# Optimization experiments

Hardware: AMD Instinct MI355X
Metric: run time of the kernel (lower is better)

Reference implementation:

```python
import jax, jax.numpy as jnp
import numpy as np

NEG_INF = -1e30

def setup_inputs() -> dict:
    key = jax.random.key(0)
    k1, k2, k3 = jax.random.split(key, 3)
    B, H, S, D = 2, 16, 2048, 128
    q = jax.random.normal(k1, (B, H, S, D), dtype=jnp.float32)
    k = jax.random.normal(k2, (B, H, S, D), dtype=jnp.float32)
    v = jax.random.normal(k3, (B, H, S, D), dtype=jnp.float32)
    return {"q": q, "k": k, "v": v}

def reference(q, k, v):
    # F.scaled_dot_product_attention(q, k, v, is_causal=True), MATH backend:
    # full score matrix, causal mask (top-left aligned: j <= i), softmax, bmm.
    D = q.shape[-1]
    scale = 1.0 / jnp.sqrt(jnp.asarray(D, dtype=q.dtype))
    scores = jnp.einsum('bhqd,bhkd->bhqk', q, k) * scale  # [B,H,S,S]
    Sq, Sk = scores.shape[-2], scores.shape[-1]
    causal = jnp.arange(Sk)[None, :] <= jnp.arange(Sq)[:, None]  # [Sq,Sk]
    scores = jnp.where(causal[None, None], scores, NEG_INF)
    attn = jax.nn.softmax(scores, axis=-1)
    return jnp.einsum('bhqk,bhkd->bhqd', attn, v)
```

## Files before the change

kernel.cpp:

```cpp
#include <hip/hip_runtime.h>
#include <cstdint>
#include <cstddef>

typedef __attribute__((ext_vector_type(8))) short short8;
typedef __attribute__((ext_vector_type(4))) float floatx4;
typedef __attribute__((ext_vector_type(2))) unsigned int uint2v;

namespace {
constexpr int kBH  = 32;
constexpr int kS   = 2048;
constexpr int kD   = 128;
constexpr int kBQ  = 64;
constexpr int kBK  = 64;
constexpr int kNQT = kS / kBQ;
constexpr int PST  = 72;
constexpr size_t kKVElems = (size_t)kBH * kS * kD;
}

__device__ __forceinline__ unsigned short f32_bf16(float f) {
    union { float f; unsigned u; } c; c.f = f;
    unsigned u = c.u;
    u += 0x7FFFu + ((u >> 16) & 1u);
    return (unsigned short)(u >> 16);
}

__device__ __forceinline__ unsigned cvt_pk_bf16(float lo, float hi) {
    unsigned r;
    asm("v_cvt_pk_bf16_f32 %0, %1, %2" : "=v"(r) : "v"(lo), "v"(hi));
    return r;
}

__device__ __forceinline__ unsigned pack_bf16x2(float lo, float hi) {
    return cvt_pk_bf16(lo, hi);
}

__device__ __forceinline__ float fast_exp2(float x) {
#if __has_builtin(__builtin_amdgcn_exp2f)
    return __builtin_amdgcn_exp2f(x);
#else
    return __expf(x * 0.6931471805599453f);
#endif
}

__device__ __forceinline__ void gl_lds16(const void* g, void* l) {
    __builtin_amdgcn_global_load_lds(
        (const __attribute__((address_space(1))) unsigned int*)g,
        (__attribute__((address_space(3))) unsigned int*)l, 16, 0, 0);
}

__global__ __launch_bounds__(256)
void prepass(const float* __restrict__ K, const float* __restrict__ V,
             unsigned short* __restrict__ Kb, unsigned short* __restrict__ Vt) {
    const int b = (int)blockIdx.x;
    const int t = (int)threadIdx.x;
    if (b < 4096) {
        const size_t i0 = ((size_t)b * 256 + t) * 8;
        floatx4 a = *(const floatx4*)(K + i0);
        floatx4 c = *(const floatx4*)(K + i0 + 4);
        union { unsigned u[4]; short8 v; } pk;
        pk.u[0] = cvt_pk_bf16(a[0], a[1]);
        pk.u[1] = cvt_pk_bf16(a[2], a[3]);
        pk.u[2] = cvt_pk_bf16(c[0], c[1]);
        pk.u[3] = cvt_pk_bf16(c[2], c[3]);
        *(short8*)(Kb + i0) = pk.v;
    } else {
        __shared__ float ldsT[64][68];
        const int vb = b - 4096;
        const int bh = vb >> 6;
        const int rem = vb & 63;
        const int s0 = (rem >> 1) * 64;
        const int d0 = (rem & 1) * 64;
        const float* vbase = V + ((size_t)bh * kS + s0) * kD + d0;
        const int sr = t >> 4, c4 = (t & 15) * 4;
#pragma unroll
        for (int p = 0; p < 4; ++p) {
            const int s = p * 16 + sr;
            *(floatx4*)&ldsT[s][c4] = *(const floatx4*)(vbase + (size_t)s * kD + c4);
        }
        __syncthreads();
        const int dr = t >> 2, sc = (t & 3) * 16;
        union { unsigned u[8]; short8 v[2]; } pk;
#pragma unroll
        for (int j = 0; j < 8; ++j)
            pk.u[j] = cvt_pk_bf16(ldsT[sc + 2 * j][dr], ldsT[sc + 2 * j + 1][dr]);
        unsigned short* out = Vt + ((size_t)(bh * kD + d0 + dr)) * kS + s0 + sc;
        *(short8*)out = pk.v[0];
        *(short8*)(out + 8) = pk.v[1];
    }
}


struct TileState {
    short8  qf[4];
    floatx4 oacc[8];
    float   lsum[4];
};

__device__ __forceinline__ void tile_step(
    TileState& ts, const unsigned short* kT, const unsigned short* vT,
    unsigned short* pw, int l16, int quad, int rowl, bool doMask)
{
    floatx4 sacc[4];
    __builtin_amdgcn_s_setprio(1);
#pragma unroll
    for (int nt = 0; nt < 4; ++nt) {
        floatx4 acc = (floatx4){0.f, 0.f, 0.f, 0.f};
#pragma unroll
        for (int ks = 0; ks < 4; ++ks) {
            short8 kf = *(const short8*)&kT[(nt * 16 + l16) * 128 + (((ks * 4 + quad) ^ l16) << 3)];
            acc = __builtin_amdgcn_mfma_f32_16x16x32_bf16(ts.qf[ks], kf, acc, 0, 0, 0);
        }
        sacc[nt] = acc;
    }
    __builtin_amdgcn_s_setprio(0);

    if (doMask) {
#pragma unroll
        for (int nt = 0; nt < 4; ++nt) {
            const int col = nt * 16 + l16;
#pragma unroll
            for (int r = 0; r < 4; ++r)
                if (col > rowl + r) sacc[nt][r] = -1e30f;
        }
    }

#pragma unroll
    for (int nt = 0; nt < 4; ++nt)
#pragma unroll
        for (int r = 0; r < 4; ++r)
            sacc[nt][r] = fast_exp2(sacc[nt][r]);
#pragma unroll
    for (int r = 0; r < 4; ++r)
        ts.lsum[r] += (sacc[0][r] + sacc[1][r]) + (sacc[2][r] + sacc[3][r]);

#pragma unroll
    for (int r = 0; r < 4; ++r) {
#pragma unroll
        for (int np = 0; np < 2; ++np) {
            const unsigned u = cvt_pk_bf16(sacc[np * 2][r], sacc[np * 2 + 1][r]);
            pw[(quad * 4 + r) * PST + (np * 2) * 16 + l16]     = (unsigned short)u;
            pw[(quad * 4 + r) * PST + (np * 2 + 1) * 16 + l16] = (unsigned short)(u >> 16);
        }
    }

    short8 pf[2];
#pragma unroll
    for (int ks = 0; ks < 2; ++ks)
        pf[ks] = *(const short8*)&pw[l16 * PST + ks * 32 + quad * 8];

    __builtin_amdgcn_s_setprio(1);
#pragma unroll
    for (int nd = 0; nd < 8; ++nd) {
        floatx4 acc = ts.oacc[nd];
#pragma unroll
        for (int ks = 0; ks < 2; ++ks) {
            short8 vf = *(const short8*)&vT[(nd * 16 + l16) * 64 + ((((ks * 4 + quad)) ^ (l16 & 7)) << 3)];
            acc = __builtin_amdgcn_mfma_f32_16x16x32_bf16(pf[ks], vf, acc, 0, 0, 0);
        }
        ts.oacc[nd] = acc;
    }
    __builtin_amdgcn_s_setprio(0);
}

__global__ __launch_bounds__(256, 2)
void fa_fwd_ws(const float* __restrict__ Qg, const unsigned short* __restrict__ Kb,
               const unsigned short* __restrict__ Vt, float* __restrict__ Og) {
    const int id = (int)blockIdx.x;
    const int qA = id >> 5;
    const int qB = kNQT - 1 - qA;
    const int bh = id & (kBH - 1);
    const int t    = (int)threadIdx.x;
    const int wave = t >> 6;
    const int lane = t & 63;
    const int quad = lane >> 4;
    const int l16  = lane & 15;
    const int rowl = wave * 16 + quad * 4;

    __shared__ __align__(16) unsigned short kT0[kBK * 128];
    __shared__ __align__(16) unsigned short kT1[kBK * 128];
    __shared__ __align__(16) unsigned short vT0[kD * 64];
    __shared__ __align__(16) unsigned short vT1[kD * 64];
    __shared__ __align__(16) unsigned short pT[4 * 16 * PST];
    unsigned short* pw = &pT[wave * 16 * PST];

    const float scale = 0.12751744459649126f;

    TileState A, B;
#pragma unroll
    for (int i = 0; i < 8; ++i) { A.oacc[i] = (floatx4){0,0,0,0}; B.oacc[i] = (floatx4){0,0,0,0}; }
#pragma unroll
    for (int r = 0; r < 4; ++r) { A.lsum[r] = 0.f; B.lsum[r] = 0.f; }

    {
        const float* qpA = Qg + ((size_t)bh * kS + qA * kBQ + wave * 16 + l16) * kD;
        const float* qpB = Qg + ((size_t)bh * kS + qB * kBQ + wave * 16 + l16) * kD;
#pragma unroll
        for (int ks = 0; ks < 4; ++ks) {
            const int d0 = ks * 32 + quad * 8;
            floatx4 a0 = *(const floatx4*)(qpA + d0);
            floatx4 a1 = *(const floatx4*)(qpA + d0 + 4);
            floatx4 b0 = *(const floatx4*)(qpB + d0);
            floatx4 b1 = *(const floatx4*)(qpB + d0 + 4);
            union { unsigned u[4]; short8 v; } pa, pb;
            pa.u[0] = cvt_pk_bf16(a0[0] * scale, a0[1] * scale);
            pa.u[1] = cvt_pk_bf16(a0[2] * scale, a0[3] * scale);
            pa.u[2] = cvt_pk_bf16(a1[0] * scale, a1[1] * scale);
            pa.u[3] = cvt_pk_bf16(a1[2] * scale, a1[3] * scale);
            pb.u[0] = cvt_pk_bf16(b0[0] * scale, b0[1] * scale);
            pb.u[1] = cvt_pk_bf16(b0[2] * scale, b0[3] * scale);
            pb.u[2] = cvt_pk_bf16(b1[0] * scale, b1[1] * scale);
            pb.u[3] = cvt_pk_bf16(b1[2] * scale, b1[3] * scale);
            A.qf[ks] = pa.v;
            B.qf[ks] = pb.v;
        }
    }

    const unsigned short* kBase = Kb + (size_t)bh * kS * kD;
    const unsigned short* vBase = Vt + (size_t)bh * kD * kS;

    auto stage = [&](int kt, unsigned short* kDst, unsigned short* vDst) {
        const int kj0 = kt * kBK;
        const int rbase = wave * 16;
#pragma unroll
        for (int i = 0; i < 4; ++i) {
            const int row = rbase + i * 4 + (lane >> 4);
            const int cg  = (lane & 15) ^ (row & 15);
            gl_lds16(kBase + ((size_t)(kj0 + row)) * kD + cg * 8,
                     &kDst[(rbase + i * 4) * 128]);
        }
        const int dbase = wave * 32;
#pragma unroll
        for (int i = 0; i < 4; ++i) {
            const int d  = dbase + i * 8 + (lane >> 3);
            const int cg = (lane & 7) ^ (d & 7);
            gl_lds16(vBase + (size_t)d * kS + kj0 + cg * 8,
                     &vDst[(dbase + i * 8) * 64]);
        }
    };

    const int last = qB;
    stage(0, kT0, vT0);
    __syncthreads();

    int kt = 0;
    for (;;) {
        if (kt < last) stage(kt + 1, kT1, vT1);
        if (kt <= qA) tile_step(A, kT0, vT0, pw, l16, quad, rowl, kt == qA);
        tile_step(B, kT0, vT0, pw, l16, quad, rowl, kt == last);
        __syncthreads();
        if (kt == last) break;
        ++kt;
        if (kt < last) stage(kt + 1, kT0, vT0);
        if (kt <= qA) tile_step(A, kT1, vT1, pw, l16, quad, rowl, kt == qA);
        tile_step(B, kT1, vT1, pw, l16, quad, rowl, kt == last);
        __syncthreads();
        if (kt == last) break;
        ++kt;
    }

#pragma unroll
    for (int tile = 0; tile < 2; ++tile) {
        TileState& ts = tile ? B : A;
        const int qt = tile ? qB : qA;
        float ls[4];
#pragma unroll
        for (int r = 0; r < 4; ++r) ls[r] = ts.lsum[r];
#pragma unroll
        for (int off = 1; off < 16; off <<= 1)
#pragma unroll
            for (int r = 0; r < 4; ++r)
                ls[r] += __shfl_xor(ls[r], off, 64);
        float inv[4];
#pragma unroll
        for (int r = 0; r < 4; ++r) inv[r] = 1.0f / ls[r];
        float* ob = Og + ((size_t)bh * kS + qt * kBQ + wave * 16 + quad * 4) * kD;
#pragma unroll
        for (int nd = 0; nd < 8; ++nd)
#pragma unroll
            for (int r = 0; r < 4; ++r)
                ob[(size_t)r * kD + nd * 16 + l16] = ts.oacc[nd][r] * inv[r];
    }
}

namespace {
constexpr int KSTf = 136;
constexpr int VSTf = 72;
}

__device__ __forceinline__ void tile_step_f(
    TileState& ts, const unsigned short* kT, const unsigned short* vT,
    unsigned short* pw, int l16, int quad, int rowl, bool doMask)
{
    floatx4 sacc[4];
    __builtin_amdgcn_s_setprio(1);
#pragma unroll
    for (int nt = 0; nt < 4; ++nt) {
        floatx4 acc = (floatx4){0.f, 0.f, 0.f, 0.f};
#pragma unroll
        for (int ks = 0; ks < 4; ++ks) {
            short8 kf = *(const short8*)&kT[(nt * 16 + l16) * KSTf + ks * 32 + quad * 8];
            acc = __builtin_amdgcn_mfma_f32_16x16x32_bf16(ts.qf[ks], kf, acc, 0, 0, 0);
        }
        sacc[nt] = acc;
    }
    __builtin_amdgcn_s_setprio(0);
    if (doMask) {
#pragma unroll
        for (int nt = 0; nt < 4; ++nt) {
            const int col = nt * 16 + l16;
#pragma unroll
            for (int r = 0; r < 4; ++r)
                if (col > rowl + r) sacc[nt][r] = -1e30f;
        }
    }
#pragma unroll
    for (int nt = 0; nt < 4; ++nt)
#pragma unroll
        for (int r = 0; r < 4; ++r)
            sacc[nt][r] = fast_exp2(sacc[nt][r]);
#pragma unroll
    for (int r = 0; r < 4; ++r)
        ts.lsum[r] += (sacc[0][r] + sacc[1][r]) + (sacc[2][r] + sacc[3][r]);
#pragma unroll
    for (int r = 0; r < 4; ++r) {
#pragma unroll
        for (int np = 0; np < 2; ++np) {
            const unsigned u = cvt_pk_bf16(sacc[np * 2][r], sacc[np * 2 + 1][r]);
            pw[(quad * 4 + r) * PST + (np * 2) * 16 + l16]     = (unsigned short)u;
            pw[(quad * 4 + r) * PST + (np * 2 + 1) * 16 + l16] = (unsigned short)(u >> 16);
        }
    }
    short8 pf[2];
#pragma unroll
    for (int ks = 0; ks < 2; ++ks)
        pf[ks] = *(const short8*)&pw[l16 * PST + ks * 32 + quad * 8];
    __builtin_amdgcn_s_setprio(1);
#pragma unroll
    for (int nd = 0; nd < 8; ++nd) {
        floatx4 acc = ts.oacc[nd];
#pragma unroll
        for (int ks = 0; ks < 2; ++ks) {
            short8 vf = *(const short8*)&vT[(nd * 16 + l16) * VSTf + ks * 32 + quad * 8];
            acc = __builtin_amdgcn_mfma_f32_16x16x32_bf16(pf[ks], vf, acc, 0, 0, 0);
        }
        ts.oacc[nd] = acc;
    }
    __builtin_amdgcn_s_setprio(0);
}

__global__ __launch_bounds__(256, 2)
void fa_fwd_fallback(const float* __restrict__ Qg, const float* __restrict__ Kg,
                     const float* __restrict__ Vg, float* __restrict__ Og) {
    const int id = (int)blockIdx.x;
    const int qA = id >> 5;
    const int qB = kNQT - 1 - qA;
    const int bh = id & (kBH - 1);
    const int t    = (int)threadIdx.x;
    const int wave = t >> 6;
    const int lane = t & 63;
    const int quad = lane >> 4;
    const int l16  = lane & 15;
    const int rowl = wave * 16 + quad * 4;

    __shared__ __align__(16) unsigned short kT[2][kBK * KSTf];
    __shared__ __align__(16) unsigned short vT[2][kD * VSTf];
    __shared__ __align__(16) unsigned short pT[4 * 16 * PST];
    unsigned short* pw = &pT[wave * 16 * PST];

    const float scale = 0.12751744459649126f;

    TileState A, B;
#pragma unroll
    for (int i = 0; i < 8; ++i) { A.oacc[i] = (floatx4){0,0,0,0}; B.oacc[i] = (floatx4){0,0,0,0}; }
#pragma unroll
    for (int r = 0; r < 4; ++r) { A.lsum[r] = 0.f; B.lsum[r] = 0.f; }
    {
        const float* qpA = Qg + ((size_t)bh * kS + qA * kBQ + wave * 16 + l16) * kD;
        const float* qpB = Qg + ((size_t)bh * kS + qB * kBQ + wave * 16 + l16) * kD;
#pragma unroll
        for (int ks = 0; ks < 4; ++ks) {
            const int d0 = ks * 32 + quad * 8;
            floatx4 a0 = *(const floatx4*)(qpA + d0);
            floatx4 a1 = *(const floatx4*)(qpA + d0 + 4);
            floatx4 b0 = *(const floatx4*)(qpB + d0);
            floatx4 b1 = *(const floatx4*)(qpB + d0 + 4);
            union { unsigned u[4]; short8 v; } pa, pb;
            pa.u[0] = cvt_pk_bf16(a0[0] * scale, a0[1] * scale);
            pa.u[1] = cvt_pk_bf16(a0[2] * scale, a0[3] * scale);
            pa.u[2] = cvt_pk_bf16(a1[0] * scale, a1[1] * scale);
            pa.u[3] = cvt_pk_bf16(a1[2] * scale, a1[3] * scale);
            pb.u[0] = cvt_pk_bf16(b0[0] * scale, b0[1] * scale);
            pb.u[1] = cvt_pk_bf16(b0[2] * scale, b0[3] * scale);
            pb.u[2] = cvt_pk_bf16(b1[0] * scale, b1[1] * scale);
            pb.u[3] = cvt_pk_bf16(b1[2] * scale, b1[3] * scale);
            A.qf[ks] = pa.v;
            B.qf[ks] = pb.v;
        }
    }

    const int kRow8 = t >> 5;
    const int kCol4 = t & 31;
    const int vD    = t & 127;
    const int vR2   = t >> 7;
    const float* kBaseH = Kg + (size_t)bh * kS * kD;
    const float* vBaseH = Vg + (size_t)bh * kS * kD;
    floatx4 kpre[8];
    float   vpreL[16], vpreH[16];

    auto issue_kv_loads = [&](int kt) {
        const float* kb = kBaseH + (size_t)(kt * kBK) * kD;
        const float* vb = vBaseH + (size_t)(kt * kBK) * kD;
#pragma unroll
        for (int p = 0; p < 8; ++p)
            kpre[p] = *(const floatx4*)(kb + (size_t)(p * 8 + kRow8) * kD + kCol4 * 4);
#pragma unroll
        for (int p = 0; p < 16; ++p) {
            const int j = p * 2 + vR2;
            vpreL[p] = vb[(size_t)(2 * j) * kD + vD];
            vpreH[p] = vb[(size_t)(2 * j + 1) * kD + vD];
        }
    };
    auto store_kv = [&](int buf) {
#pragma unroll
        for (int p = 0; p < 8; ++p) {
            union { unsigned u[2]; uint2v v; } w;
            w.u[0] = cvt_pk_bf16(kpre[p][0], kpre[p][1]);
            w.u[1] = cvt_pk_bf16(kpre[p][2], kpre[p][3]);
            *(uint2v*)&kT[buf][(p * 8 + kRow8) * KSTf + kCol4 * 4] = w.v;
        }
#pragma unroll
        for (int p = 0; p < 16; ++p) {
            const int j = p * 2 + vR2;
            *(unsigned*)&vT[buf][vD * VSTf + 2 * j] = pack_bf16x2(vpreL[p], vpreH[p]);
        }
    };

    const int last = qB;
    issue_kv_loads(0);
    store_kv(0);
    __syncthreads();
    for (int kt = 0; kt <= last; ++kt) {
        const int buf = kt & 1;
        if (kt < last) issue_kv_loads(kt + 1);
        if (kt <= qA) tile_step_f(A, kT[buf], vT[buf], pw, l16, quad, rowl, kt == qA);
        tile_step_f(B, kT[buf], vT[buf], pw, l16, quad, rowl, kt == last);
        if (kt < last) {
            store_kv(buf ^ 1);
            __syncthreads();
        }
    }
#pragma unroll
    for (int tile = 0; tile < 2; ++tile) {
        TileState& ts = tile ? B : A;
        const int qt = tile ? qB : qA;
        float ls[4];
#pragma unroll
        for (int r = 0; r < 4; ++r) ls[r] = ts.lsum[r];
#pragma unroll
        for (int off = 1; off < 16; off <<= 1)
#pragma unroll
            for (int r = 0; r < 4; ++r)
                ls[r] += __shfl_xor(ls[r], off, 64);
        float inv[4];
#pragma unroll
        for (int r = 0; r < 4; ++r) inv[r] = 1.0f / ls[r];
        float* ob = Og + ((size_t)bh * kS + qt * kBQ + wave * 16 + quad * 4) * kD;
#pragma unroll
        for (int nd = 0; nd < 8; ++nd)
#pragma unroll
            for (int r = 0; r < 4; ++r)
                ob[(size_t)r * kD + nd * 16 + l16] = ts.oacc[nd][r] * inv[r];
    }
}

extern "C" void kernel_launch(void* const* d_in, const int* in_sizes, int n_in,
                              void* d_out, int out_size, void* d_ws, size_t ws_size,
                              hipStream_t stream) {
    (void)in_sizes; (void)n_in; (void)out_size;
    const float* q = (const float*)d_in[0];
    const float* k = (const float*)d_in[1];
    const float* v = (const float*)d_in[2];
    float* o = (float*)d_out;
    const size_t need = 2 * kKVElems * sizeof(unsigned short);
    if (ws_size >= need) {
        unsigned short* Kb = (unsigned short*)d_ws;
        unsigned short* Vt = Kb + kKVElems;
        prepass<<<dim3(4096 + 2048), 256, 0, stream>>>(k, v, Kb, Vt);
        fa_fwd_ws<<<dim3((kNQT / 2) * kBH), 256, 0, stream>>>(q, Kb, Vt, o);
    } else {
        fa_fwd_fallback<<<dim3((kNQT / 2) * kBH), 256, 0, stream>>>(q, k, v, o);
    }
}
```

Before: 177.5 us.

## Transpose S MFMA and pass P through registers via bpermute, fuse dual tiles

Swaps the MFMA operands in the QK^T product so each lane holds one query row's scores. The P matrix then moves into the PV operand layout with ds_bpermute instead of a write and read through LDS, and the per-row sum reduction collapses to one scalar per lane. It also adds a dual-tile step that shares K and V fragment loads between the two query tiles, and remaps the block-to-head assignment. The cost is extra bpermute and select instructions plus higher register pressure from keeping two tiles' scores live under 2-block occupancy.

Measured after the change: 179.8 us. About the same (+1.3%).

```diff
diff --git a/kernel.cpp b/kernel.cpp
--- a/kernel.cpp
+++ b/kernel.cpp
@@ -93,12 +93,32 @@
 struct TileState {
     short8  qf[4];
     floatx4 oacc[8];
-    float   lsum[4];
+    float   lsum;
 };
+
+__device__ __forceinline__ short8 p_gather(unsigned pe0, unsigned pe1,
+                                           unsigned po0, unsigned po1,
+                                           int lane, int prm_lo, int prm_hi) {
+    int ce0 = __builtin_amdgcn_ds_bpermute(prm_lo, (int)pe0);
+    int ce1 = __builtin_amdgcn_ds_bpermute(prm_lo, (int)pe1);
+    int ce2 = __builtin_amdgcn_ds_bpermute(prm_hi, (int)pe0);
+    int ce3 = __builtin_amdgcn_ds_bpermute(prm_hi, (int)pe1);
+    int co0 = __builtin_amdgcn_ds_bpermute(prm_lo, (int)po0);
+    int co1 = __builtin_amdgcn_ds_bpermute(prm_lo, (int)po1);
+    int co2 = __builtin_amdgcn_ds_bpermute(prm_hi, (int)po0);
+    int co3 = __builtin_amdgcn_ds_bpermute(prm_hi, (int)po1);
+    const bool hi = lane >= 32;
+    union { unsigned u[4]; short8 v; } r;
+    r.u[0] = hi ? (unsigned)co0 : (unsigned)ce0;
+    r.u[1] = hi ? (unsigned)co1 : (unsigned)ce1;
+    r.u[2] = hi ? (unsigned)co2 : (unsigned)ce2;
+    r.u[3] = hi ? (unsigned)co3 : (unsigned)ce3;
+    return r.v;
+}
 
 __device__ __forceinline__ void tile_step(
     TileState& ts, const unsigned short* kT, const unsigned short* vT,
-    unsigned short* pw, int l16, int quad, int rowl, bool doMask)
+    int lane, int l16, int quad, int rowq, int prm_lo, int prm_hi, bool doMask)
 {
     floatx4 sacc[4];
     __builtin_amdgcn_s_setprio(1);
@@ -108,45 +128,33 @@
 #pragma unroll
         for (int ks = 0; ks < 4; ++ks) {
             short8 kf = *(const short8*)&kT[(nt * 16 + l16) * 128 + (((ks * 4 + quad) ^ l16) << 3)];
-            acc = __builtin_amdgcn_mfma_f32_16x16x32_bf16(ts.qf[ks], kf, acc, 0, 0, 0);
+            acc = __builtin_amdgcn_mfma_f32_16x16x32_bf16(kf, ts.qf[ks], acc, 0, 0, 0);
         }
         sacc[nt] = acc;
     }
     __builtin_amdgcn_s_setprio(0);
 
-    if (doMask) {
-#pragma unroll
-        for (int nt = 0; nt < 4; ++nt) {
-            const int col = nt * 16 + l16;
-#pragma unroll
-            for (int r = 0; r < 4; ++r)
-                if (col > rowl + r) sacc[nt][r] = -1e30f;
-        }
-    }
-
+    float lsum = 0.f;
 #pragma unroll
     for (int nt = 0; nt < 4; ++nt)
 #pragma unroll
-        for (int r = 0; r < 4; ++r)
-            sacc[nt][r] = fast_exp2(sacc[nt][r]);
-#pragma unroll
-    for (int r = 0; r < 4; ++r)
-        ts.lsum[r] += (sacc[0][r] + sacc[1][r]) + (sacc[2][r] + sacc[3][r]);
-
-#pragma unroll
-    for (int r = 0; r < 4; ++r) {
-#pragma unroll
-        for (int np = 0; np < 2; ++np) {
-            const unsigned u = cvt_pk_bf16(sacc[np * 2][r], sacc[np * 2 + 1][r]);
-            pw[(quad * 4 + r) * PST + (np * 2) * 16 + l16]     = (unsigned short)u;
-            pw[(quad * 4 + r) * PST + (np * 2 + 1) * 16 + l16] = (unsigned short)(u >> 16);
-        }
-    }
-
+        for (int r = 0; r < 4; ++r) {
+            float e = fast_exp2(sacc[nt][r]);
+            if (doMask && (nt * 16 + quad * 4 + r > rowq)) e = 0.f;
+            sacc[nt][r] = e;
+            lsum += e;
+        }
+    ts.lsum += lsum;
+
+    unsigned pk[4][2];
+#pragma unroll
+    for (int nt = 0; nt < 4; ++nt) {
+        pk[nt][0] = cvt_pk_bf16(sacc[nt][0], sacc[nt][1]);
+        pk[nt][1] = cvt_pk_bf16(sacc[nt][2], sacc[nt][3]);
+    }
     short8 pf[2];
-#pragma unroll
-    for (int ks = 0; ks < 2; ++ks)
-        pf[ks] = *(const short8*)&pw[l16 * PST + ks * 32 + quad * 8];
+    pf[0] = p_gather(pk[0][0], pk[0][1], pk[1][0], pk[1][1], lane, prm_lo, prm_hi);
+    pf[1] = p_gather(pk[2][0], pk[2][1], pk[3][0], pk[3][1], lane, prm_lo, prm_hi);
 
     __builtin_amdgcn_s_setprio(1);
 #pragma unroll
@@ -158,6 +166,72 @@
             acc = __builtin_amdgcn_mfma_f32_16x16x32_bf16(pf[ks], vf, acc, 0, 0, 0);
         }
         ts.oacc[nd] = acc;
+    }
+    __builtin_amdgcn_s_setprio(0);
+}
+
+__device__ __forceinline__ void tile_step_dual(
+    TileState& A, TileState& B, const unsigned short* kT, const unsigned short* vT,
+    int lane, int l16, int quad, int rowq, int prm_lo, int prm_hi, bool maskA)
+{
+    floatx4 saccA[4], saccB[4];
+    __builtin_amdgcn_s_setprio(1);
+#pragma unroll
+    for (int nt = 0; nt < 4; ++nt) {
+        floatx4 accA = (floatx4){0.f, 0.f, 0.f, 0.f};
+        floatx4 accB = (floatx4){0.f, 0.f, 0.f, 0.f};
+#pragma unroll
+        for (int ks = 0; ks < 4; ++ks) {
+            short8 kf = *(const short8*)&kT[(nt * 16 + l16) * 128 + (((ks * 4 + quad) ^ l16) << 3)];
+            accA = __builtin_amdgcn_mfma_f32_16x16x32_bf16(kf, A.qf[ks], accA, 0, 0, 0);
+            accB = __builtin_amdgcn_mfma_f32_16x16x32_bf16(kf, B.qf[ks], accB, 0, 0, 0);
+        }
+        saccA[nt] = accA;
+        saccB[nt] = accB;
+    }
+    __builtin_amdgcn_s_setprio(0);
+
+    float lsA = 0.f, lsB = 0.f;
+#pragma unroll
+    for (int nt = 0; nt < 4; ++nt)
+#pragma unroll
+        for (int r = 0; r < 4; ++r) {
+            float ea = fast_exp2(saccA[nt][r]);
+            float eb = fast_exp2(saccB[nt][r]);
+            if (maskA && (nt * 16 + quad * 4 + r > rowq)) ea = 0.f;
+            saccA[nt][r] = ea; lsA += ea;
+            saccB[nt][r] = eb; lsB += eb;
+        }
+    A.lsum += lsA;
+    B.lsum += lsB;
+
+    unsigned pkA[4][2], pkB[4][2];
+#pragma unroll
+    for (int nt = 0; nt < 4; ++nt) {
+        pkA[nt][0] = cvt_pk_bf16(saccA[nt][0], saccA[nt][1]);
+        pkA[nt][1] = cvt_pk_bf16(saccA[nt][2], saccA[nt][3]);
+        pkB[nt][0] = cvt_pk_bf16(saccB[nt][0], saccB[nt][1]);
+        pkB[nt][1] = cvt_pk_bf16(saccB[nt][2], saccB[nt][3]);
+    }
+    short8 pfA[2], pfB[2];
+    pfA[0] = p_gather(pkA[0][0], pkA[0][1], pkA[1][0], pkA[1][1], lane, prm_lo, prm_hi);
+    pfA[1] = p_gather(pkA[2][0], pkA[2][1], pkA[3][0], pkA[3][1], lane, prm_lo, prm_hi);
+    pfB[0] = p_gather(pkB[0][0], pkB[0][1], pkB[1][0], pkB[1][1], lane, prm_lo, prm_hi);
+    pfB[1] = p_gather(pkB[2][0], pkB[2][1], pkB[3][0], pkB[3][1], lane, prm_lo, prm_hi);
+
+    __builtin_amdgcn_s_setprio(1);
+#pragma unroll
+    for (int nd = 0; nd < 8; ++nd) {
+        floatx4 accA = A.oacc[nd];
+        floatx4 accB = B.oacc[nd];
+#pragma unroll
+        for (int ks = 0; ks < 2; ++ks) {
+            short8 vf = *(const short8*)&vT[(nd * 16 + l16) * 64 + ((((ks * 4 + quad)) ^ (l16 & 7)) << 3)];
+            accA = __builtin_amdgcn_mfma_f32_16x16x32_bf16(pfA[ks], vf, accA, 0, 0, 0);
+            accB = __builtin_amdgcn_mfma_f32_16x16x32_bf16(pfB[ks], vf, accB, 0, 0, 0);
+        }
+        A.oacc[nd] = accA;
+        B.oacc[nd] = accB;
     }
     __builtin_amdgcn_s_setprio(0);
 }
@@ -168,28 +242,27 @@
     const int id = (int)blockIdx.x;
     const int qA = id >> 5;
     const int qB = kNQT - 1 - qA;
-    const int bh = id & (kBH - 1);
+    const int bh = (id & 7) * 4 + ((id >> 3) & 3);
     const int t    = (int)threadIdx.x;
     const int wave = t >> 6;
     const int lane = t & 63;
     const int quad = lane >> 4;
     const int l16  = lane & 15;
-    const int rowl = wave * 16 + quad * 4;
+    const int rowq = wave * 16 + l16;
+    const int prm_lo = (((lane >> 4) & 1) << 7) + (l16 << 2);
+    const int prm_hi = prm_lo + 64;
 
     __shared__ __align__(16) unsigned short kT0[kBK * 128];
     __shared__ __align__(16) unsigned short kT1[kBK * 128];
     __shared__ __align__(16) unsigned short vT0[kD * 64];
     __shared__ __align__(16) unsigned short vT1[kD * 64];
-    __shared__ __align__(16) unsigned short pT[4 * 16 * PST];
-    unsigned short* pw = &pT[wave * 16 * PST];
 
     const float scale = 0.12751744459649126f;
 
     TileState A, B;
 #pragma unroll
     for (int i = 0; i < 8; ++i) { A.oacc[i] = (floatx4){0,0,0,0}; B.oacc[i] = (floatx4){0,0,0,0}; }
-#pragma unroll
-    for (int r = 0; r < 4; ++r) { A.lsum[r] = 0.f; B.lsum[r] = 0.f; }
+    A.lsum = 0.f; B.lsum = 0.f;
 
     {
         const float* qpA = Qg + ((size_t)bh * kS + qA * kBQ + wave * 16 + l16) * kD;
@@ -245,14 +318,14 @@
     int kt = 0;
     for (;;) {
         if (kt < last) stage(kt + 1, kT1, vT1);
-        if (kt <= qA) tile_step(A, kT0, vT0, pw, l16, quad, rowl, kt == qA);
-        tile_step(B, kT0, vT0, pw, l16, quad, rowl, kt == last);
+        if (kt <= qA) tile_step_dual(A, B, kT0, vT0, lane, l16, quad, rowq, prm_lo, prm_hi, kt == qA);
+        else          tile_step(B, kT0, vT0, lane, l16, quad, rowq, prm_lo, prm_hi, kt == last);
         __syncthreads();
         if (kt == last) break;
         ++kt;
         if (kt < last) stage(kt + 1, kT0, vT0);
-        if (kt <= qA) tile_step(A, kT1, vT1, pw, l16, quad, rowl, kt == qA);
-        tile_step(B, kT1, vT1, pw, l16, quad, rowl, kt == last);
+        if (kt <= qA) tile_step_dual(A, B, kT1, vT1, lane, l16, quad, rowq, prm_lo, prm_hi, kt == qA);
+        else          tile_step(B, kT1, vT1, lane, l16, quad, rowq, prm_lo, prm_hi, kt == last);
         __syncthreads();
         if (kt == last) break;
         ++kt;
@@ -262,17 +335,13 @@
     for (int tile = 0; tile < 2; ++tile) {
         TileState& ts = tile ? B : A;
         const int qt = tile ? qB : qA;
-        float ls[4];
-#pragma unroll
-        for (int r = 0; r < 4; ++r) ls[r] = ts.lsum[r];
-#pragma unroll
-        for (int off = 1; off < 16; off <<= 1)
-#pragma unroll
-            for (int r = 0; r < 4; ++r)
-                ls[r] += __shfl_xor(ls[r], off, 64);
+        float rs = ts.lsum;
+        rs += __shfl_xor(rs, 16, 64);
+        rs += __shfl_xor(rs, 32, 64);
         float inv[4];
 #pragma unroll
-        for (int r = 0; r < 4; ++r) inv[r] = 1.0f / ls[r];
+        for (int r = 0; r < 4; ++r)
+            inv[r] = 1.0f / __shfl(rs, quad * 4 + r, 64);
         float* ob = Og + ((size_t)bh * kS + qt * kBQ + wave * 16 + quad * 4) * kD;
 #pragma unroll
         for (int nd = 0; nd < 8; ++nd)
@@ -287,8 +356,14 @@
 constexpr int VSTf = 72;
 }
 
+struct TileStateF {
+    short8  qf[4];
+    floatx4 oacc[8];
+    float   lsum[4];
+};
+
 __device__ __forceinline__ void tile_step_f(
-    TileState& ts, const unsigned short* kT, const unsigned short* vT,
+    TileStateF& ts, const unsigned short* kT, const unsigned short* vT,
     unsigned short* pw, int l16, int quad, int rowl, bool doMask)
 {
     floatx4 sacc[4];
@@ -369,7 +444,7 @@
 
     const float scale = 0.12751744459649126f;
 
-    TileState A, B;
+    TileStateF A, B;
 #pragma unroll
     for (int i = 0; i < 8; ++i) { A.oacc[i] = (floatx4){0,0,0,0}; B.oacc[i] = (floatx4){0,0,0,0}; }
 #pragma unroll
@@ -451,7 +526,7 @@
     }
 #pragma unroll
     for (int tile = 0; tile < 2; ++tile) {
-        TileState& ts = tile ? B : A;
+        TileStateF& ts = tile ? B : A;
         const int qt = tile ? qB : qA;
         float ls[4];
 #pragma unroll
```

## Give each block one query tile with 32-key tiles and register-permuted P

Applied to the files above, without the earlier changes.

The main attention kernel now gives each block a single 64-row query tile instead of a paired short/long tile, doubling the grid and raising launch bounds to 4 blocks per CU. Blocks are ordered so long and short causal tiles interleave. Keys are processed in 32-wide tiles with transposed score MFMAs. The probability matrix is repacked to the PV operand layout with ds_bpermute rather than an LDS round trip. This aims for better occupancy and load balance and less LDS traffic, at the cost of more tile iterations and barriers, and K/V being re-read by more blocks.

Result: slower. 186.5 us (+5.1%).

```diff
diff --git a/kernel.cpp b/kernel.cpp
--- a/kernel.cpp
+++ b/kernel.cpp
@@ -11,7 +11,7 @@
 constexpr int kS   = 2048;
 constexpr int kD   = 128;
 constexpr int kBQ  = 64;
-constexpr int kBK  = 64;
+constexpr int kBK  = 32;
 constexpr int kNQT = kS / kBQ;
 constexpr int PST  = 72;
 constexpr size_t kKVElems = (size_t)kBH * kS * kD;
@@ -90,14 +90,180 @@
 }
 
 
-struct TileState {
+__global__ __launch_bounds__(256, 4)
+void fa_fwd_ws(const float* __restrict__ Qg, const unsigned short* __restrict__ Kb,
+               const unsigned short* __restrict__ Vt, float* __restrict__ Og) {
+    const int id = (int)blockIdx.x;
+    const int s  = id >> 8;
+    const int j  = id & 255;
+    const int bh = (j & 7) * 4 + ((j >> 3) & 3);
+    const int a  = j >> 5;
+    const int qt = (s == 0) ? a : (s == 1) ? (31 - a) : (s == 2) ? (8 + a) : (23 - a);
+
+    const int t    = (int)threadIdx.x;
+    const int wave = t >> 6;
+    const int lane = t & 63;
+    const int quad = lane >> 4;
+    const int l16  = lane & 15;
+    const int rowq_base = qt * 64 + wave * 16 + l16;
+    const int prm_lo = ((quad & 1) << 7) + (l16 << 2);
+    const int prm_hi = prm_lo + 64;
+    const bool hi = lane >= 32;
+
+    __shared__ __align__(16) unsigned short kT0[kBK * 128];
+    __shared__ __align__(16) unsigned short kT1[kBK * 128];
+    __shared__ __align__(16) unsigned short vT0[kD * kBK];
+    __shared__ __align__(16) unsigned short vT1[kD * kBK];
+
+    const float scale = 0.12751744459649126f;
+
+    short8  qf[4];
+    floatx4 oacc[8];
+    float   lsum = 0.f;
+#pragma unroll
+    for (int i = 0; i < 8; ++i) oacc[i] = (floatx4){0, 0, 0, 0};
+
+    {
+        const float* qp = Qg + ((size_t)bh * kS + rowq_base) * kD;
+#pragma unroll
+        for (int ks = 0; ks < 4; ++ks) {
+            const int d0 = ks * 32 + quad * 8;
+            floatx4 a0 = *(const floatx4*)(qp + d0);
+            floatx4 a1 = *(const floatx4*)(qp + d0 + 4);
+            union { unsigned u[4]; short8 v; } pa;
+            pa.u[0] = cvt_pk_bf16(a0[0] * scale, a0[1] * scale);
+            pa.u[1] = cvt_pk_bf16(a0[2] * scale, a0[3] * scale);
+            pa.u[2] = cvt_pk_bf16(a1[0] * scale, a1[1] * scale);
+            pa.u[3] = cvt_pk_bf16(a1[2] * scale, a1[3] * scale);
+            qf[ks] = pa.v;
+        }
+    }
+
+    const unsigned short* kBase = Kb + (size_t)bh * kS * kD;
+    const unsigned short* vBase = Vt + (size_t)bh * kD * kS;
+
+    auto stage = [&](int kt, unsigned short* kDst, unsigned short* vDst) {
+        const int kj0 = kt * kBK;
+#pragma unroll
+        for (int i = 0; i < 2; ++i) {
+            const int rbase = wave * 8 + i * 4;
+            const int row = rbase + (lane >> 4);
+            const int cg  = (lane & 15) ^ (row & 15);
+            gl_lds16(kBase + ((size_t)(kj0 + row)) * kD + cg * 8,
+                     &kDst[rbase * 128]);
+        }
+#pragma unroll
+        for (int i = 0; i < 2; ++i) {
+            const int dbase = wave * 32 + i * 16;
+            const int d  = dbase + (lane >> 2);
+            const int cg = (lane & 3) ^ ((d >> 1) & 3);
+            gl_lds16(vBase + (size_t)d * kS + kj0 + cg * 8,
+                     &vDst[dbase * kBK]);
+        }
+    };
+
+    auto tile_step = [&](const unsigned short* kT, const unsigned short* vT,
+                         bool doMask, int rq) {
+        floatx4 sacc[2];
+        __builtin_amdgcn_s_setprio(1);
+#pragma unroll
+        for (int nt = 0; nt < 2; ++nt) {
+            floatx4 acc = (floatx4){0.f, 0.f, 0.f, 0.f};
+#pragma unroll
+            for (int ks = 0; ks < 4; ++ks) {
+                short8 kf = *(const short8*)&kT[(nt * 16 + l16) * 128 + (((ks * 4 + quad) ^ l16) << 3)];
+                acc = __builtin_amdgcn_mfma_f32_16x16x32_bf16(kf, qf[ks], acc, 0, 0, 0);
+            }
+            sacc[nt] = acc;
+        }
+        __builtin_amdgcn_s_setprio(0);
+
+        float ls = 0.f;
+#pragma unroll
+        for (int nt = 0; nt < 2; ++nt)
+#pragma unroll
+            for (int r = 0; r < 4; ++r) {
+                float e = fast_exp2(sacc[nt][r]);
+                if (doMask && (nt * 16 + quad * 4 + r > rq)) e = 0.f;
+                sacc[nt][r] = e;
+                ls += e;
+            }
+        lsum += ls;
+
+        unsigned pk0a = cvt_pk_bf16(sacc[0][0], sacc[0][1]);
+        unsigned pk0b = cvt_pk_bf16(sacc[0][2], sacc[0][3]);
+        unsigned pk1a = cvt_pk_bf16(sacc[1][0], sacc[1][1]);
+        unsigned pk1b = cvt_pk_bf16(sacc[1][2], sacc[1][3]);
+        int e0 = __builtin_amdgcn_ds_bpermute(prm_lo, (int)pk0a);
+        int e1 = __builtin_amdgcn_ds_bpermute(prm_lo, (int)pk0b);
+        int e2 = __builtin_amdgcn_ds_bpermute(prm_hi, (int)pk0a);
+        int e3 = __builtin_amdgcn_ds_bpermute(prm_hi, (int)pk0b);
+        int o0 = __builtin_amdgcn_ds_bpermute(prm_lo, (int)pk1a);
+        int o1 = __builtin_amdgcn_ds_bpermute(prm_lo, (int)pk1b);
+        int o2 = __builtin_amdgcn_ds_bpermute(prm_hi, (int)pk1a);
+        int o3 = __builtin_amdgcn_ds_bpermute(prm_hi, (int)pk1b);
+        union { unsigned u[4]; short8 v; } pf;
+        pf.u[0] = hi ? (unsigned)o0 : (unsigned)e0;
+        pf.u[1] = hi ? (unsigned)o1 : (unsigned)e1;
+        pf.u[2] = hi ? (unsigned)o2 : (unsigned)e2;
+        pf.u[3] = hi ? (unsigned)o3 : (unsigned)e3;
+
+        __builtin_amdgcn_s_setprio(1);
+#pragma unroll
+        for (int nd = 0; nd < 8; ++nd) {
+            short8 vf = *(const short8*)&vT[(nd * 16 + l16) * kBK + ((quad ^ ((l16 >> 1) & 3)) << 3)];
+            oacc[nd] = __builtin_amdgcn_mfma_f32_16x16x32_bf16(pf.v, vf, oacc[nd], 0, 0, 0);
+        }
+        __builtin_amdgcn_s_setprio(0);
+    };
+
+    const int last = 2 * qt + 1;
+    stage(0, kT0, vT0);
+    __syncthreads();
+
+    int kt = 0;
+    for (;;) {
+        if (kt < last) stage(kt + 1, kT1, vT1);
+        tile_step(kT0, vT0, kt >= 2 * qt, rowq_base - kt * kBK);
+        __syncthreads();
+        if (kt == last) break;
+        ++kt;
+        if (kt < last) stage(kt + 1, kT0, vT0);
+        tile_step(kT1, vT1, kt >= 2 * qt, rowq_base - kt * kBK);
+        __syncthreads();
+        if (kt == last) break;
+        ++kt;
+    }
+
+    float rs = lsum;
+    rs += __shfl_xor(rs, 16, 64);
+    rs += __shfl_xor(rs, 32, 64);
+    float inv[4];
+#pragma unroll
+    for (int r = 0; r < 4; ++r)
+        inv[r] = 1.0f / __shfl(rs, quad * 4 + r, 64);
+    float* ob = Og + ((size_t)bh * kS + qt * 64 + wave * 16 + quad * 4) * kD;
+#pragma unroll
+    for (int nd = 0; nd < 8; ++nd)
+#pragma unroll
+        for (int r = 0; r < 4; ++r)
+            ob[(size_t)r * kD + nd * 16 + l16] = oacc[nd][r] * inv[r];
+}
+
+namespace {
+constexpr int kBKf = 64;
+constexpr int KSTf = 136;
+constexpr int VSTf = 72;
+}
+
+struct TileStateF {
     short8  qf[4];
     floatx4 oacc[8];
     float   lsum[4];
 };
 
-__device__ __forceinline__ void tile_step(
-    TileState& ts, const unsigned short* kT, const unsigned short* vT,
+__device__ __forceinline__ void tile_step_f(
+    TileStateF& ts, const unsigned short* kT, const unsigned short* vT,
     unsigned short* pw, int l16, int quad, int rowl, bool doMask)
 {
     floatx4 sacc[4];
@@ -107,13 +273,12 @@
         floatx4 acc = (floatx4){0.f, 0.f, 0.f, 0.f};
 #pragma unroll
         for (int ks = 0; ks < 4; ++ks) {
-            short8 kf = *(const short8*)&kT[(nt * 16 + l16) * 128 + (((ks * 4 + quad) ^ l16) << 3)];
+            short8 kf = *(const short8*)&kT[(nt * 16 + l16) * KSTf + ks * 32 + quad * 8];
             acc = __builtin_amdgcn_mfma_f32_16x16x32_bf16(ts.qf[ks], kf, acc, 0, 0, 0);
         }
         sacc[nt] = acc;
     }
     __builtin_amdgcn_s_setprio(0);
-
     if (doMask) {
 #pragma unroll
         for (int nt = 0; nt < 4; ++nt) {
@@ -123,7 +288,6 @@
                 if (col > rowl + r) sacc[nt][r] = -1e30f;
         }
     }
-
 #pragma unroll
     for (int nt = 0; nt < 4; ++nt)
 #pragma unroll
@@ -132,7 +296,6 @@
 #pragma unroll
     for (int r = 0; r < 4; ++r)
         ts.lsum[r] += (sacc[0][r] + sacc[1][r]) + (sacc[2][r] + sacc[3][r]);
-
 #pragma unroll
     for (int r = 0; r < 4; ++r) {
 #pragma unroll
@@ -142,19 +305,17 @@
             pw[(quad * 4 + r) * PST + (np * 2 + 1) * 16 + l16] = (unsigned short)(u >> 16);
         }
     }
-
     short8 pf[2];
 #pragma unroll
     for (int ks = 0; ks < 2; ++ks)
         pf[ks] = *(const short8*)&pw[l16 * PST + ks * 32 + quad * 8];
-
     __builtin_amdgcn_s_setprio(1);
 #pragma unroll
     for (int nd = 0; nd < 8; ++nd) {
         floatx4 acc = ts.oacc[nd];
 #pragma unroll
         for (int ks = 0; ks < 2; ++ks) {
-            short8 vf = *(const short8*)&vT[(nd * 16 + l16) * 64 + ((((ks * 4 + quad)) ^ (l16 & 7)) << 3)];
+            short8 vf = *(const short8*)&vT[(nd * 16 + l16) * VSTf + ks * 32 + quad * 8];
             acc = __builtin_amdgcn_mfma_f32_16x16x32_bf16(pf[ks], vf, acc, 0, 0, 0);
         }
         ts.oacc[nd] = acc;
@@ -163,8 +324,8 @@
 }
 
 __global__ __launch_bounds__(256, 2)
-void fa_fwd_ws(const float* __restrict__ Qg, const unsigned short* __restrict__ Kb,
-               const unsigned short* __restrict__ Vt, float* __restrict__ Og) {
+void fa_fwd_fallback(const float* __restrict__ Qg, const float* __restrict__ Kg,
+                     const float* __restrict__ Vg, float* __restrict__ Og) {
     const int id = (int)blockIdx.x;
     const int qA = id >> 5;
     const int qB = kNQT - 1 - qA;
@@ -176,21 +337,18 @@
     const int l16  = lane & 15;
     const int rowl = wave * 16 + quad * 4;
 
-    __shared__ __align__(16) unsigned short kT0[kBK * 128];
-    __shared__ __align__(16) unsigned short kT1[kBK * 128];
-    __shared__ __align__(16) unsigned short vT0[kD * 64];
-    __shared__ __align__(16) unsigned short vT1[kD * 64];
+    __shared__ __align__(16) unsigned short kT[2][kBKf * KSTf];
+    __shared__ __align__(16) unsigned short vT[2][kD * VSTf];
     __shared__ __align__(16) unsigned short pT[4 * 16 * PST];
     unsigned short* pw = &pT[wave * 16 * PST];
 
     const float scale = 0.12751744459649126f;
 
-    TileState A, B;
+    TileStateF A, B;
 #pragma unroll
     for (int i = 0; i < 8; ++i) { A.oacc[i] = (floatx4){0,0,0,0}; B.oacc[i] = (floatx4){0,0,0,0}; }
 #pragma unroll
     for (int r = 0; r < 4; ++r) { A.lsum[r] = 0.f; B.lsum[r] = 0.f; }
-
     {
         const float* qpA = Qg + ((size_t)bh * kS + qA * kBQ + wave * 16 + l16) * kD;
         const float* qpB = Qg + ((size_t)bh * kS + qB * kBQ + wave * 16 + l16) * kD;
@@ -215,189 +373,6 @@
         }
     }
 
-    const unsigned short* kBase = Kb + (size_t)bh * kS * kD;
-    const unsigned short* vBase = Vt + (size_t)bh * kD * kS;
-
-    auto stage = [&](int kt, unsigned short* kDst, unsigned short* vDst) {
-        const int kj0 = kt * kBK;
-        const int rbase = wave * 16;
-#pragma unroll
-        for (int i = 0; i < 4; ++i) {
-            const int row = rbase + i * 4 + (lane >> 4);
-            const int cg  = (lane & 15) ^ (row & 15);
-            gl_lds16(kBase + ((size_t)(kj0 + row)) * kD + cg * 8,
-                     &kDst[(rbase + i * 4) * 128]);
-        }
-        const int dbase = wave * 32;
-#pragma unroll
-        for (int i = 0; i < 4; ++i) {
-            const int d  = dbase + i * 8 + (lane >> 3);
-            const int cg = (lane & 7) ^ (d & 7);
-            gl_lds16(vBase + (size_t)d * kS + kj0 + cg * 8,
-                     &vDst[(dbase + i * 8) * 64]);
-        }
-    };
-
-    const int last = qB;
-    stage(0, kT0, vT0);
-    __syncthreads();
-
-    int kt = 0;
-    for (;;) {
-        if (kt < last) stage(kt + 1, kT1, vT1);
-        if (kt <= qA) tile_step(A, kT0, vT0, pw, l16, quad, rowl, kt == qA);
-        tile_step(B, kT0, vT0, pw, l16, quad, rowl, kt == last);
-        __syncthreads();
-        if (kt == last) break;
-        ++kt;
-        if (kt < last) stage(kt + 1, kT0, vT0);
-        if (kt <= qA) tile_step(A, kT1, vT1, pw, l16, quad, rowl, kt == qA);
-        tile_step(B, kT1, vT1, pw, l16, quad, rowl, kt == last);
-        __syncthreads();
-        if (kt == last) break;
-        ++kt;
-    }
-
-#pragma unroll
-    for (int tile = 0; tile < 2; ++tile) {
-        TileState& ts = tile ? B : A;
-        const int qt = tile ? qB : qA;
-        float ls[4];
-#pragma unroll
-        for (int r = 0; r < 4; ++r) ls[r] = ts.lsum[r];
-#pragma unroll
-        for (int off = 1; off < 16; off <<= 1)
-#pragma unroll
-            for (int r = 0; r < 4; ++r)
-                ls[r] += __shfl_xor(ls[r], off, 64);
-        float inv[4];
-#pragma unroll
-        for (int r = 0; r < 4; ++r) inv[r] = 1.0f / ls[r];
-        float* ob = Og + ((size_t)bh * kS + qt * kBQ + wave * 16 + quad * 4) * kD;
-#pragma unroll
-        for (int nd = 0; nd < 8; ++nd)
-#pragma unroll
-            for (int r = 0; r < 4; ++r)
-                ob[(size_t)r * kD + nd * 16 + l16] = ts.oacc[nd][r] * inv[r];
-    }
-}
-
-namespace {
-constexpr int KSTf = 136;
-constexpr int VSTf = 72;
-}
-
-__device__ __forceinline__ void tile_step_f(
-    TileState& ts, const unsigned short* kT, const unsigned short* vT,
-    unsigned short* pw, int l16, int quad, int rowl, bool doMask)
-{
-    floatx4 sacc[4];
-    __builtin_amdgcn_s_setprio(1);
-#pragma unroll
-    for (int nt = 0; nt < 4; ++nt) {
-        floatx4 acc = (floatx4){0.f, 0.f, 0.f, 0.f};
-#pragma unroll
-        for (int ks = 0; ks < 4; ++ks) {
-            short8 kf = *(const short8*)&kT[(nt * 16 + l16) * KSTf + ks * 32 + quad * 8];
-            acc = __builtin_amdgcn_mfma_f32_16x16x32_bf16(ts.qf[ks], kf, acc, 0, 0, 0);
-        }
-        sacc[nt] = acc;
-    }
-    __builtin_amdgcn_s_setprio(0);
-    if (doMask) {
-#pragma unroll
-        for (int nt = 0; nt < 4; ++nt) {
-            const int col = nt * 16 + l16;
-#pragma unroll
-            for (int r = 0; r < 4; ++r)
-                if (col > rowl + r) sacc[nt][r] = -1e30f;
-        }
-    }
-#pragma unroll
-    for (int nt = 0; nt < 4; ++nt)
-#pragma unroll
-        for (int r = 0; r < 4; ++r)
-            sacc[nt][r] = fast_exp2(sacc[nt][r]);
-#pragma unroll
-    for (int r = 0; r < 4; ++r)
-        ts.lsum[r] += (sacc[0][r] + sacc[1][r]) + (sacc[2][r] + sacc[3][r]);
-#pragma unroll
-    for (int r = 0; r < 4; ++r) {
-#pragma unroll
-        for (int np = 0; np < 2; ++np) {
-            const unsigned u = cvt_pk_bf16(sacc[np * 2][r], sacc[np * 2 + 1][r]);
-            pw[(quad * 4 + r) * PST + (np * 2) * 16 + l16]     = (unsigned short)u;
-            pw[(quad * 4 + r) * PST + (np * 2 + 1) * 16 + l16] = (unsigned short)(u >> 16);
-        }
-    }
-    short8 pf[2];
-#pragma unroll
-    for (int ks = 0; ks < 2; ++ks)
-        pf[ks] = *(const short8*)&pw[l16 * PST + ks * 32 + quad * 8];
-    __builtin_amdgcn_s_setprio(1);
-#pragma unroll
-    for (int nd = 0; nd < 8; ++nd) {
-        floatx4 acc = ts.oacc[nd];
-#pragma unroll
-        for (int ks = 0; ks < 2; ++ks) {
-            short8 vf = *(const short8*)&vT[(nd * 16 + l16) * VSTf + ks * 32 + quad * 8];
-            acc = __builtin_amdgcn_mfma_f32_16x16x32_bf16(pf[ks], vf, acc, 0, 0, 0);
-        }
-        ts.oacc[nd] = acc;
-    }
-    __builtin_amdgcn_s_setprio(0);
-}
-
-__global__ __launch_bounds__(256, 2)
-void fa_fwd_fallback(const float* __restrict__ Qg, const float* __restrict__ Kg,
-                     const float* __restrict__ Vg, float* __restrict__ Og) {
-    const int id = (int)blockIdx.x;
-    const int qA = id >> 5;
-    const int qB = kNQT - 1 - qA;
-    const int bh = id & (kBH - 1);
-    const int t    = (int)threadIdx.x;
-    const int wave = t >> 6;
-    const int lane = t & 63;
-    const int quad = lane >> 4;
-    const int l16  = lane & 15;
-    const int rowl = wave * 16 + quad * 4;
-
-    __shared__ __align__(16) unsigned short kT[2][kBK * KSTf];
-    __shared__ __align__(16) unsigned short vT[2][kD * VSTf];
-    __shared__ __align__(16) unsigned short pT[4 * 16 * PST];
-    unsigned short* pw = &pT[wave * 16 * PST];
-
-    const float scale = 0.12751744459649126f;
-
-    TileState A, B;
-#pragma unroll
-    for (int i = 0; i < 8; ++i) { A.oacc[i] = (floatx4){0,0,0,0}; B.oacc[i] = (floatx4){0,0,0,0}; }
-#pragma unroll
-    for (int r = 0; r < 4; ++r) { A.lsum[r] = 0.f; B.lsum[r] = 0.f; }
-    {
-        const float* qpA = Qg + ((size_t)bh * kS + qA * kBQ + wave * 16 + l16) * kD;
-        const float* qpB = Qg + ((size_t)bh * kS + qB * kBQ + wave * 16 + l16) * kD;
-#pragma unroll
-        for (int ks = 0; ks < 4; ++ks) {
-            const int d0 = ks * 32 + quad * 8;
-            floatx4 a0 = *(const floatx4*)(qpA + d0);
-            floatx4 a1 = *(const floatx4*)(qpA + d0 + 4);
-            floatx4 b0 = *(const floatx4*)(qpB + d0);
-            floatx4 b1 = *(const floatx4*)(qpB + d0 + 4);
-            union { unsigned u[4]; short8 v; } pa, pb;
-            pa.u[0] = cvt_pk_bf16(a0[0] * scale, a0[1] * scale);
-            pa.u[1] = cvt_pk_bf16(a0[2] * scale, a0[3] * scale);
-            pa.u[2] = cvt_pk_bf16(a1[0] * scale, a1[1] * scale);
-            pa.u[3] = cvt_pk_bf16(a1[2] * scale, a1[3] * scale);
-            pb.u[0] = cvt_pk_bf16(b0[0] * scale, b0[1] * scale);
-            pb.u[1] = cvt_pk_bf16(b0[2] * scale, b0[3] * scale);
-            pb.u[2] = cvt_pk_bf16(b1[0] * scale, b1[1] * scale);
-            pb.u[3] = cvt_pk_bf16(b1[2] * scale, b1[3] * scale);
-            A.qf[ks] = pa.v;
-            B.qf[ks] = pb.v;
-        }
-    }
-
     const int kRow8 = t >> 5;
     const int kCol4 = t & 31;
     const int vD    = t & 127;
@@ -408,8 +383,8 @@
     float   vpreL[16], vpreH[16];
 
     auto issue_kv_loads = [&](int kt) {
-        const float* kb = kBaseH + (size_t)(kt * kBK) * kD;
-        const float* vb = vBaseH + (size_t)(kt * kBK) * kD;
+        const float* kb = kBaseH + (size_t)(kt * kBKf) * kD;
+        const float* vb = vBaseH + (size_t)(kt * kBKf) * kD;
 #pragma unroll
         for (int p = 0; p < 8; ++p)
             kpre[p] = *(const floatx4*)(kb + (size_t)(p * 8 + kRow8) * kD + kCol4 * 4);
@@ -451,7 +426,7 @@
     }
 #pragma unroll
     for (int tile = 0; tile < 2; ++tile) {
-        TileState& ts = tile ? B : A;
+        TileStateF& ts = tile ? B : A;
         const int qt = tile ? qB : qA;
         float ls[4];
 #pragma unroll
@@ -486,7 +461,7 @@
         unsigned short* Kb = (unsigned short*)d_ws;
         unsigned short* Vt = Kb + kKVElems;
         prepass<<<dim3(4096 + 2048), 256, 0, stream>>>(k, v, Kb, Vt);
-        fa_fwd_ws<<<dim3((kNQT / 2) * kBH), 256, 0, stream>>>(q, Kb, Vt, o);
+        fa_fwd_ws<<<dim3(kNQT * kBH), 256, 0, stream>>>(q, Kb, Vt, o);
     } else {
         fa_fwd_fallback<<<dim3((kNQT / 2) * kBH), 256, 0, stream>>>(q, k, v, o);
     }
```
